# Performance work log

Measured on AMD Instinct MI355X. Metric: run time of the kernel, lower is better.

## Reference

```python
import jax, jax.numpy as jnp
import numpy as np


def setup_inputs() -> dict:
    key = jax.random.key(0)
    ks = jax.random.split(key, 6)
    B, L, D, H, U = 256, 225, 1280, 256, 256
    features = jax.random.normal(ks[0], (B, L, D), dtype=jnp.float32)
    hidden = jax.random.normal(ks[1], (B, H), dtype=jnp.float32)
    W1 = jax.random.normal(ks[2], (D, U), dtype=jnp.float32) * (1.0 / np.sqrt(D))
    b1 = jnp.zeros((U,), dtype=jnp.float32)
    W2 = jax.random.normal(ks[3], (H, U), dtype=jnp.float32) * (1.0 / np.sqrt(H))
    b2 = jnp.zeros((U,), dtype=jnp.float32)
    V = jax.random.normal(ks[4], (U, 1), dtype=jnp.float32) * (1.0 / np.sqrt(U))
    bV = jnp.zeros((1,), dtype=jnp.float32)
    return {"features": features, "hidden": hidden, "W1": W1, "b1": b1,
            "W2": W2, "b2": b2, "V": V, "bV": bV}


def reference(features, hidden, W1, b1, W2, b2, V, bV):
    # features: [B, L, D]; hidden: [B, H]
    proj_f = jnp.einsum('bld,du->blu', features, W1) + b1        # [B, L, U]
    proj_h = (hidden @ W2 + b2)[:, None, :]                      # [B, 1, U]
    score = jnp.tanh(proj_f + proj_h)                            # [B, L, U]
    logits = jnp.einsum('blu,uo->blo', score, V) + bV            # [B, L, 1]
    attn = jax.nn.softmax(logits, axis=1)                        # [B, L, 1]
    context = jnp.sum(attn * features, axis=1)                   # [B, D]
    return context
```

## Files before the change

kernel.cpp:

```cpp
#include <hip/hip_runtime.h>
#include <hip/hip_bf16.h>

#define B_ 256
#define L_ 225
#define D_ 1280
#define H_ 256
#define U_ 256
#define LT 45
#define LTP 48

typedef __bf16  bf16x8 __attribute__((ext_vector_type(8)));
typedef float   f32x4  __attribute__((ext_vector_type(4)));
typedef unsigned short u16x8 __attribute__((ext_vector_type(8)));
typedef unsigned short u16x4 __attribute__((ext_vector_type(4)));

__device__ __forceinline__ unsigned short f2bf(float f) {
    union { __hip_bfloat16 h; unsigned short u; } cv;
    cv.h = __float2bfloat16(f);
    return cv.u;
}

__device__ __forceinline__ f32x4 bf4_to_f32(u16x4 w) {
    union { unsigned u; float f; } a0, a1, a2, a3;
    a0.u = (unsigned)w[0] << 16; a1.u = (unsigned)w[1] << 16;
    a2.u = (unsigned)w[2] << 16; a3.u = (unsigned)w[3] << 16;
    return (f32x4){a0.f, a1.f, a2.f, a3.f};
}

__device__ __forceinline__ float wredsum(float x) {
#pragma unroll
    for (int off = 32; off > 0; off >>= 1) x += __shfl_xor(x, off, 64);
    return x;
}

__global__ void k_prep_w1t(const float* __restrict__ W1, __hip_bfloat16* __restrict__ w1t) {
    int idx = blockIdx.x * 256 + threadIdx.x;
    int k = idx / U_;
    int u = idx % U_;
    w1t[(size_t)u * D_ + k] = __float2bfloat16(W1[idx]);
}

__global__ void k_proj_h(const float* __restrict__ hidden, const float* __restrict__ W2,
                         const float* __restrict__ b1, const float* __restrict__ b2,
                         float* __restrict__ ph) {
    __shared__ float sh[H_];
    int b = blockIdx.x;
    int u = threadIdx.x;
    sh[u] = hidden[b * H_ + u];
    __syncthreads();
    float acc = b1[u] + b2[u];
#pragma unroll 8
    for (int h = 0; h < H_; ++h) acc += sh[h] * W2[h * U_ + u];
    ph[b * U_ + u] = acc;
}

__global__ __launch_bounds__(512) void k_fused(
        const float* __restrict__ feat,
        const __hip_bfloat16* __restrict__ w1t,
        const float* __restrict__ ph,
        const float* __restrict__ Vv,
        float* __restrict__ num,
        float* __restrict__ den) {
    __shared__ __align__(128) char smem[159424];
    char*  sB  = smem + 122880;
    float* sV  = (float*)(smem + 155648);
    float* sPh = (float*)(smem + 156672);
    float* sL  = (float*)(smem + 157696);
    float* sW  = (float*)(smem + 159232);

    const int tid  = threadIdx.x;
    const int lane = tid & 63;
    const int wave = tid >> 6;
    const int blk  = blockIdx.x;
    const int b    = blk / 5;
    const int s5   = blk - b * 5;
    const int l0   = s5 * LT;

    if (tid < 256) { sV[tid] = Vv[tid]; sPh[tid] = ph[b * 256 + tid]; }

    const float* featB = feat + ((size_t)b * L_ + l0) * D_;

#pragma unroll
    for (int p = 0; p < 15; ++p) {
        int id  = p * 512 + tid;
        int row = id / 160;
        int c8  = id - row * 160;
        int rc  = row < LT ? row : (LT - 1);
        const float* src = featB + (size_t)rc * D_ + c8 * 8;
        f32x4 v0 = *reinterpret_cast<const f32x4*>(src);
        f32x4 v1 = *reinterpret_cast<const f32x4*>(src + 4);
        u16x8 w;
        w[0] = f2bf(v0[0]); w[1] = f2bf(v0[1]); w[2] = f2bf(v0[2]); w[3] = f2bf(v0[3]);
        w[4] = f2bf(v1[0]); w[5] = f2bf(v1[1]); w[6] = f2bf(v1[2]); w[7] = f2bf(v1[3]);
        *reinterpret_cast<u16x8*>(smem + row * 2560 + ((c8 * 16) ^ ((row & 7) << 4))) = w;
    }

    const __hip_bfloat16* bSrc[4];
    int bDst[4];
#pragma unroll
    for (int pass = 0; pass < 4; ++pass) {
        int sI  = pass * 512 + tid;
        int u   = sI >> 3;
        int c8s = sI & 7;
        int c8g = c8s ^ (u & 7);
        bSrc[pass] = w1t + (size_t)u * D_ + c8g * 8;
        bDst[pass] = sI * 16;
    }
    u16x8 breg[4];
#pragma unroll
    for (int pass = 0; pass < 4; ++pass)
        breg[pass] = *reinterpret_cast<const u16x8*>(bSrc[pass]);

    f32x4 acc[3][2];
#pragma unroll
    for (int mi = 0; mi < 3; ++mi)
#pragma unroll
        for (int ni = 0; ni < 2; ++ni)
            acc[mi][ni] = (f32x4){0.f, 0.f, 0.f, 0.f};

    const int u0   = wave * 32 + (lane & 15);
    const int bswz0 = (u0 & 7) << 4;
    const int bswz1 = ((u0 + 16) & 7) << 4;
    __syncthreads();

    for (int kt = 0; kt < 20; ++kt) {
#pragma unroll
        for (int pass = 0; pass < 4; ++pass)
            *reinterpret_cast<u16x8*>(sB + bDst[pass]) = breg[pass];
        if (kt < 19) {
#pragma unroll
            for (int pass = 0; pass < 4; ++pass)
                breg[pass] = *reinterpret_cast<const u16x8*>(bSrc[pass] + (kt + 1) * 64);
        }
        __syncthreads();
#pragma unroll
        for (int ks = 0; ks < 2; ++ks) {
            const int kloc = ks * 64 + ((lane >> 4) << 4);
            bf16x8 a[3], bb[2];
#pragma unroll
            for (int mi = 0; mi < 3; ++mi) {
                int r = mi * 16 + (lane & 15);
                a[mi] = *reinterpret_cast<const bf16x8*>(
                    smem + r * 2560 + ((kt * 128 + kloc) ^ ((r & 7) << 4)));
            }
            bb[0] = *reinterpret_cast<const bf16x8*>(sB + u0 * 128 + (kloc ^ bswz0));
            bb[1] = *reinterpret_cast<const bf16x8*>(sB + (u0 + 16) * 128 + (kloc ^ bswz1));
#pragma unroll
            for (int mi = 0; mi < 3; ++mi)
#pragma unroll
                for (int ni = 0; ni < 2; ++ni)
                    acc[mi][ni] = __builtin_amdgcn_mfma_f32_16x16x32_bf16(
                        a[mi], bb[ni], acc[mi][ni], 0, 0, 0);
        }
        __syncthreads();
    }

    float ph0 = sPh[u0], ph1 = sPh[u0 + 16];
    float v0  = sV[u0],  v1  = sV[u0 + 16];
#pragma unroll
    for (int mi = 0; mi < 3; ++mi) {
#pragma unroll
        for (int rg = 0; rg < 4; ++rg) {
            int row = mi * 16 + ((lane >> 4) << 2) + rg;
            float x0 = acc[mi][0][rg] + ph0;
            float x1 = acc[mi][1][rg] + ph1;
            float sl = (1.f - 2.f / (__expf(2.f * x0) + 1.f)) * v0
                     + (1.f - 2.f / (__expf(2.f * x1) + 1.f)) * v1;
            sl += __shfl_xor(sl, 1, 64);
            sl += __shfl_xor(sl, 2, 64);
            sl += __shfl_xor(sl, 4, 64);
            sl += __shfl_xor(sl, 8, 64);
            if ((lane & 15) == 0) sL[wave * LTP + row] = sl;
        }
    }
    __syncthreads();

    if (wave == 0) {
        float w = 0.f;
        if (lane < LT) {
            float lg = 0.f;
#pragma unroll
            for (int wc = 0; wc < 8; ++wc) lg += sL[wc * LTP + lane];
            w = __expf(lg);
            sW[lane] = w;
        }
        float d = wredsum(w);
        if (lane == 0) den[blk] = d;
    }
    __syncthreads();

    f32x4 c[5];
#pragma unroll
    for (int ch = 0; ch < 5; ++ch) c[ch] = (f32x4){0.f, 0.f, 0.f, 0.f};
    for (int l = wave; l < LT; l += 8) {
        float wgt = sW[l];
        const char* arow = smem + l * 2560;
        int rswz = (l & 7) << 4;
#pragma unroll
        for (int ch = 0; ch < 5; ++ch) {
            u16x4 w4 = *reinterpret_cast<const u16x4*>(
                arow + ((ch * 512 + lane * 8) ^ rswz));
            c[ch] += wgt * bf4_to_f32(w4);
        }
    }
    __syncthreads();

    float* pc = (float*)smem;
#pragma unroll
    for (int ch = 0; ch < 5; ++ch)
        *reinterpret_cast<f32x4*>(pc + wave * 1280 + ch * 256 + (lane << 2)) = c[ch];
    __syncthreads();
    if (tid < 320) {
        f32x4 s = (f32x4){0.f, 0.f, 0.f, 0.f};
#pragma unroll
        for (int w = 0; w < 8; ++w)
            s += *reinterpret_cast<const f32x4*>(pc + w * 1280 + (tid << 2));
        *reinterpret_cast<f32x4*>(num + (size_t)blk * 1280 + (tid << 2)) = s;
    }
}

__global__ void k_combine(const float* __restrict__ num, const float* __restrict__ den,
                          float* __restrict__ out) {
    int b = blockIdx.x;
    int t = threadIdx.x;
    f32x4 n = (f32x4){0.f, 0.f, 0.f, 0.f};
    float d = 0.f;
#pragma unroll
    for (int s = 0; s < 5; ++s) {
        n += *reinterpret_cast<const f32x4*>(num + (size_t)(b * 5 + s) * 1280 + (t << 2));
        d += den[b * 5 + s];
    }
    n *= (1.f / d);
    *reinterpret_cast<f32x4*>(out + (size_t)b * D_ + (t << 2)) = n;
}

extern "C" void kernel_launch(void* const* d_in, const int* in_sizes, int n_in,
                              void* d_out, int out_size, void* d_ws, size_t ws_size,
                              hipStream_t stream) {
    const float* feat   = (const float*)d_in[0];
    const float* hidden = (const float*)d_in[1];
    const float* W1     = (const float*)d_in[2];
    const float* b1     = (const float*)d_in[3];
    const float* W2     = (const float*)d_in[4];
    const float* b2     = (const float*)d_in[5];
    const float* Vv     = (const float*)d_in[6];

    char* ws = (char*)d_ws;
    __hip_bfloat16* w1t = (__hip_bfloat16*)(ws);
    float* ph  = (float*)(ws + 655360);
    float* num = (float*)(ws + 917504);
    float* den = (float*)(ws + 7471104);
    float* out = (float*)d_out;

    k_prep_w1t<<<(U_ * D_) / 256, 256, 0, stream>>>(W1, w1t);
    k_proj_h  <<<B_, U_, 0, stream>>>(hidden, W2, b1, b2, ph);
    k_fused   <<<B_ * 5, 512, 0, stream>>>(feat, w1t, ph, Vv, num, den);
    k_combine <<<B_, 320, 0, stream>>>(num, den, out);
}
```

Before: 147.0 us.

## Stream feature tiles through double-buffered LDS and reread fp32 features for context

Instead of staging the whole 45x1280 bf16 feature tile in LDS, the kernel now streams 64-wide K slices of features and W1 through double-buffered LDS. W1 is loaded with global_load_lds directly into shared memory, and the next slice's loads overlap the current MFMA step. This cuts LDS use roughly in half, so more blocks can be resident per CU. The price is that the weighted context sum must reread the fp32 features from global memory or cache rather than LDS. The context is now computed from fp32 features instead of bf16 copies, which changes numerics slightly.

```diff
diff --git a/kernel.cpp b/kernel.cpp
--- a/kernel.cpp
+++ b/kernel.cpp
@@ -2,6 +2,8 @@
 #include <hip/hip_bf16.h>
 
 #define B_ 256
+#define L_ 1225
+#undef L_
 #define L_ 225
 #define D_ 1280
 #define H_ 256
@@ -12,7 +14,6 @@
 typedef __bf16  bf16x8 __attribute__((ext_vector_type(8)));
 typedef float   f32x4  __attribute__((ext_vector_type(4)));
 typedef unsigned short u16x8 __attribute__((ext_vector_type(8)));
-typedef unsigned short u16x4 __attribute__((ext_vector_type(4)));
 
 __device__ __forceinline__ unsigned short f2bf(float f) {
     union { __hip_bfloat16 h; unsigned short u; } cv;
@@ -20,11 +21,11 @@
     return cv.u;
 }
 
-__device__ __forceinline__ f32x4 bf4_to_f32(u16x4 w) {
-    union { unsigned u; float f; } a0, a1, a2, a3;
-    a0.u = (unsigned)w[0] << 16; a1.u = (unsigned)w[1] << 16;
-    a2.u = (unsigned)w[2] << 16; a3.u = (unsigned)w[3] << 16;
-    return (f32x4){a0.f, a1.f, a2.f, a3.f};
+__device__ __forceinline__ void gload_lds16(const void* g, void* l) {
+    __builtin_amdgcn_global_load_lds(
+        (const __attribute__((address_space(1))) unsigned int*)g,
+        (__attribute__((address_space(3))) unsigned int*)l,
+        16, 0, 0);
 }
 
 __device__ __forceinline__ float wredsum(float x) {
@@ -54,19 +55,16 @@
     ph[b * U_ + u] = acc;
 }
 
-__global__ __launch_bounds__(512) void k_fused(
+__global__ __launch_bounds__(512, 4) void k_fused(
         const float* __restrict__ feat,
         const __hip_bfloat16* __restrict__ w1t,
         const float* __restrict__ ph,
         const float* __restrict__ Vv,
         float* __restrict__ num,
         float* __restrict__ den) {
-    __shared__ __align__(128) char smem[159424];
-    char*  sB  = smem + 122880;
-    float* sV  = (float*)(smem + 155648);
-    float* sPh = (float*)(smem + 156672);
-    float* sL  = (float*)(smem + 157696);
-    float* sW  = (float*)(smem + 159232);
+    __shared__ __align__(128) char smem[79552];
+    float* sL = (float*)(smem + 77824);
+    float* sW = (float*)(smem + 79360);
 
     const int tid  = threadIdx.x;
     const int lane = tid & 63;
@@ -76,24 +74,14 @@
     const int s5   = blk - b * 5;
     const int l0   = s5 * LT;
 
-    if (tid < 256) { sV[tid] = Vv[tid]; sPh[tid] = ph[b * 256 + tid]; }
-
     const float* featB = feat + ((size_t)b * L_ + l0) * D_;
 
-#pragma unroll
-    for (int p = 0; p < 15; ++p) {
-        int id  = p * 512 + tid;
-        int row = id / 160;
-        int c8  = id - row * 160;
-        int rc  = row < LT ? row : (LT - 1);
-        const float* src = featB + (size_t)rc * D_ + c8 * 8;
-        f32x4 v0 = *reinterpret_cast<const f32x4*>(src);
-        f32x4 v1 = *reinterpret_cast<const f32x4*>(src + 4);
-        u16x8 w;
-        w[0] = f2bf(v0[0]); w[1] = f2bf(v0[1]); w[2] = f2bf(v0[2]); w[3] = f2bf(v0[3]);
-        w[4] = f2bf(v1[0]); w[5] = f2bf(v1[1]); w[6] = f2bf(v1[2]); w[7] = f2bf(v1[3]);
-        *reinterpret_cast<u16x8*>(smem + row * 2560 + ((c8 * 16) ^ ((row & 7) << 4))) = w;
-    }
+    const int ar   = tid >> 3;
+    const int arc  = ar < LT ? ar : (LT - 1);
+    const int ac8  = tid & 7;
+    const bool aAct = (tid < 384);
+    const float* aSrc0 = featB + (size_t)arc * D_ + ac8 * 8;
+    const int aOff = ar * 128 + ((ac8 * 16) ^ ((ar & 7) << 4));
 
     const __hip_bfloat16* bSrc[4];
     int bDst[4];
@@ -106,10 +94,6 @@
         bSrc[pass] = w1t + (size_t)u * D_ + c8g * 8;
         bDst[pass] = sI * 16;
     }
-    u16x8 breg[4];
-#pragma unroll
-    for (int pass = 0; pass < 4; ++pass)
-        breg[pass] = *reinterpret_cast<const u16x8*>(bSrc[pass]);
 
     f32x4 acc[3][2];
 #pragma unroll
@@ -118,33 +102,43 @@
         for (int ni = 0; ni < 2; ++ni)
             acc[mi][ni] = (f32x4){0.f, 0.f, 0.f, 0.f};
 
-    const int u0   = wave * 32 + (lane & 15);
-    const int bswz0 = (u0 & 7) << 4;
-    const int bswz1 = ((u0 + 16) & 7) << 4;
-    __syncthreads();
-
-    for (int kt = 0; kt < 20; ++kt) {
+    const int u0 = wave * 32 + (lane & 15);
+
+    auto loadA = [&](int kt, f32x4* v) {
+        if (aAct) {
+            const float* src = aSrc0 + kt * 64;
+            v[0] = *reinterpret_cast<const f32x4*>(src);
+            v[1] = *reinterpret_cast<const f32x4*>(src + 4);
+        }
+    };
+    auto storeA = [&](const f32x4* v, char* bufA) {
+        if (aAct) {
+            u16x8 w;
+            w[0] = f2bf(v[0][0]); w[1] = f2bf(v[0][1]); w[2] = f2bf(v[0][2]); w[3] = f2bf(v[0][3]);
+            w[4] = f2bf(v[1][0]); w[5] = f2bf(v[1][1]); w[6] = f2bf(v[1][2]); w[7] = f2bf(v[1][3]);
+            *reinterpret_cast<u16x8*>(bufA + aOff) = w;
+        }
+    };
+    auto stageB = [&](int kt, char* bufB) {
 #pragma unroll
         for (int pass = 0; pass < 4; ++pass)
-            *reinterpret_cast<u16x8*>(sB + bDst[pass]) = breg[pass];
-        if (kt < 19) {
-#pragma unroll
-            for (int pass = 0; pass < 4; ++pass)
-                breg[pass] = *reinterpret_cast<const u16x8*>(bSrc[pass] + (kt + 1) * 64);
-        }
-        __syncthreads();
+            gload_lds16(bSrc[pass] + kt * 64, bufB + bDst[pass]);
+    };
+    auto compute = [&](const char* bufA, const char* bufB) {
 #pragma unroll
         for (int ks = 0; ks < 2; ++ks) {
-            const int kloc = ks * 64 + ((lane >> 4) << 4);
+            const int kk2 = (ks * 32 + ((lane >> 4) << 3)) * 2;
             bf16x8 a[3], bb[2];
 #pragma unroll
             for (int mi = 0; mi < 3; ++mi) {
                 int r = mi * 16 + (lane & 15);
                 a[mi] = *reinterpret_cast<const bf16x8*>(
-                    smem + r * 2560 + ((kt * 128 + kloc) ^ ((r & 7) << 4)));
+                    bufA + r * 128 + (kk2 ^ ((r & 7) << 4)));
             }
-            bb[0] = *reinterpret_cast<const bf16x8*>(sB + u0 * 128 + (kloc ^ bswz0));
-            bb[1] = *reinterpret_cast<const bf16x8*>(sB + (u0 + 16) * 128 + (kloc ^ bswz1));
+            bb[0] = *reinterpret_cast<const bf16x8*>(
+                bufB + u0 * 128 + (kk2 ^ ((u0 & 7) << 4)));
+            bb[1] = *reinterpret_cast<const bf16x8*>(
+                bufB + (u0 + 16) * 128 + (kk2 ^ (((u0 + 16) & 7) << 4)));
 #pragma unroll
             for (int mi = 0; mi < 3; ++mi)
 #pragma unroll
@@ -152,11 +146,31 @@
                     acc[mi][ni] = __builtin_amdgcn_mfma_f32_16x16x32_bf16(
                         a[mi], bb[ni], acc[mi][ni], 0, 0, 0);
         }
+    };
+
+    {
+        f32x4 v[2];
+        loadA(0, v);
+        stageB(0, smem + 12288);
+        storeA(v, smem);
+    }
+    __syncthreads();
+    int cur = 0;
+    for (int kt = 0; kt < 20; ++kt) {
+        f32x4 v[2];
+        if (kt < 19) {
+            loadA(kt + 1, v);
+            stageB(kt + 1, smem + 12288 + (cur ^ 1) * 32768);
+        }
+        compute(smem + cur * 6144, smem + 12288 + cur * 32768);
+        if (kt < 19) storeA(v, smem + (cur ^ 1) * 6144);
         __syncthreads();
-    }
-
-    float ph0 = sPh[u0], ph1 = sPh[u0 + 16];
-    float v0  = sV[u0],  v1  = sV[u0 + 16];
+        cur ^= 1;
+    }
+
+    const float* phB = ph + b * 256;
+    float ph0 = phB[u0], ph1 = phB[u0 + 16];
+    float v0  = Vv[u0],  v1  = Vv[u0 + 16];
 #pragma unroll
     for (int mi = 0; mi < 3; ++mi) {
 #pragma unroll
@@ -194,14 +208,10 @@
     for (int ch = 0; ch < 5; ++ch) c[ch] = (f32x4){0.f, 0.f, 0.f, 0.f};
     for (int l = wave; l < LT; l += 8) {
         float wgt = sW[l];
-        const char* arow = smem + l * 2560;
-        int rswz = (l & 7) << 4;
-#pragma unroll
-        for (int ch = 0; ch < 5; ++ch) {
-            u16x4 w4 = *reinterpret_cast<const u16x4*>(
-                arow + ((ch * 512 + lane * 8) ^ rswz));
-            c[ch] += wgt * bf4_to_f32(w4);
-        }
+        const float* fr = featB + (size_t)l * D_ + (lane << 2);
+#pragma unroll
+        for (int ch = 0; ch < 5; ++ch)
+            c[ch] += wgt * *reinterpret_cast<const f32x4*>(fr + ch * 256);
     }
     __syncthreads();
 
```

New measurement: 152.9 us. 1.04x slower.
